# Kernel tuning notes

Measured on AMD Instinct MI355X. Metric: run time of the kernel, lower is better.

Reference implementation:

```python
import jax, jax.numpy as jnp
import numpy as np

B, N, D = 8, 128, 256
EPS = 1e-5


def _layernorm(x, g, b):
    m = jnp.mean(x, axis=-1, keepdims=True)
    v = jnp.mean(jnp.square(x - m), axis=-1, keepdims=True)
    return (x - m) * jax.lax.rsqrt(v + EPS) * g + b


def setup_inputs() -> dict:
    key = jax.random.key(0)
    ks = jax.random.split(key, 24)
    s = 0.05  # param init scale
    return {
        "text": jax.random.normal(ks[0], (B, N, D), jnp.float32),
        "adj1": jax.random.uniform(ks[1], (B, N, N), jnp.float32),
        "adj2": jax.random.uniform(ks[2], (B, N, N), jnp.float32),
        "edge1": jax.random.normal(ks[3], (B, N, N, D), jnp.float32) * 0.1,
        "edge2": jax.random.normal(ks[4], (B, N, N, D), jnp.float32) * 0.1,
        "textmask": jnp.ones((B, N), jnp.float32),
        "weight": jax.random.normal(ks[5], (D, D), jnp.float32) * s,
        "bias": jax.random.normal(ks[6], (D,), jnp.float32) * s,
        "gamma": jnp.ones((D,), jnp.float32),
        "beta": jnp.zeros((D,), jnp.float32),
        "fuse1_w": jax.random.normal(ks[7], (2 * D, D), jnp.float32) * s,
        "fuse2_w": jax.random.normal(ks[8], (2 * D, D), jnp.float32) * s,
        "fc3_w": jax.random.normal(ks[9], (2 * D, D), jnp.float32) * s,
        "fc1_w0": jax.random.normal(ks[10], (3 * D, D), jnp.float32) * s,
        "fc1_w1": jax.random.normal(ks[11], (D, 1), jnp.float32) * s,
        "fc1_b1": jnp.zeros((1,), jnp.float32),
        "fc2_w0": jax.random.normal(ks[12], (3 * D, D), jnp.float32) * s,
        "fc2_w1": jax.random.normal(ks[13], (D, 1), jnp.float32) * s,
        "fc2_b1": jnp.zeros((1,), jnp.float32),
        "align_lin": jax.random.normal(ks[14], (D, D), jnp.float32) * s,
        "align_bias": jax.random.normal(ks[15], (D,), jnp.float32) * s,
    }


def reference(text, adj1, adj2, edge1, edge2, textmask, weight, bias, gamma,
              beta, fuse1_w, fuse2_w, fc3_w, fc1_w0, fc1_w1, fc1_b1,
              fc2_w0, fc2_w1, fc2_b1, align_lin, align_bias):
    d = text.shape[-1]
    # ---- SelfAlignment ----
    logits = jnp.einsum('bid,bjd->bij', text @ align_lin, text)
    mask_add = (1.0 - textmask)[:, None, :] * -1e20
    probs = jax.nn.softmax(logits + mask_add, axis=-1)
    outss = jnp.einsum('bij,bjd->bid', probs, text) * textmask[..., None] + align_bias

    # ---- GCN body ----
    out = jax.nn.relu(text @ weight)  # [B,N,D]

    # edge contributions are loop-invariant: precompute once
    # torch cat([x,e]) @ W  ==  x @ W[:d] + e @ W[d:]
    e1_fuse = jnp.einsum('bijd,de->bije', edge1, fuse1_w[d:])
    e2_fuse = jnp.einsum('bijd,de->bije', edge2, fuse2_w[d:])
    e1_fc = jnp.einsum('bijd,de->bije', edge1, fc1_w0[2 * d:])
    e2_fc = jnp.einsum('bijd,de->bije', edge2, fc2_w0[2 * d:])

    denom1 = jnp.sum(adj1, axis=2, keepdims=True) + 1.0  # [B,N,1]
    denom2 = jnp.sum(adj2, axis=2, keepdims=True) + 1.0

    for _ in range(3):  # K = 3
        # text1[b,i,j] = out[b,i]; text2[b,i,j] = out[b,j]
        t_i1 = (out @ fc1_w0[:d])[:, :, None, :]        # text1 part, fc1
        t_j1 = (out @ fc1_w0[d:2 * d])[:, None, :, :]   # text2 part, fc1
        t_i2 = (out @ fc2_w0[:d])[:, :, None, :]
        t_j2 = (out @ fc2_w0[d:2 * d])[:, None, :, :]

        teout = jax.nn.relu((out @ fuse1_w[:d])[:, None, :, :] + e1_fuse)  # [B,N,N,D]
        tein = jax.nn.relu((out @ fuse2_w[:d])[:, None, :, :] + e2_fuse)

        s1 = jax.nn.sigmoid(jax.nn.relu(t_i1 + t_j1 + e1_fc) @ fc1_w1 + fc1_b1)[..., 0]  # [B,N,N]
        s2 = jax.nn.sigmoid(jax.nn.relu(t_i2 + t_j2 + e2_fc) @ fc2_w1 + fc2_b1)[..., 0]

        out1 = jnp.einsum('bij,bijd->bid', adj1 * s1, teout) / denom1
        out2 = jnp.einsum('bij,bijd->bid', adj2 * s2, tein) / denom2

        out = jax.nn.relu(out1 @ fc3_w[:d] + out2 @ fc3_w[d:]) + out + bias
        out = _layernorm(out, gamma, beta)  # dropout = identity (eval)
    return out, outss
```

## Files before the change

kernel.cpp:

```cpp
#include <hip/hip_runtime.h>

typedef unsigned short u16;
typedef unsigned int u32;
typedef __attribute__((ext_vector_type(8))) short bf16x8;
typedef __attribute__((ext_vector_type(4))) float f32x4;
typedef __attribute__((ext_vector_type(16))) float f32x16;

__device__ __forceinline__ u16 f2bf(float f) {
  u32 u = __float_as_uint(f);
  return (u16)((u + 0x7fffu + ((u >> 16) & 1u)) >> 16);
}
__device__ __forceinline__ float bf2f(u16 h) {
  return __uint_as_float(((u32)h) << 16);
}

__device__ __forceinline__ void glds16(const void* g, void* l) {
  __builtin_amdgcn_global_load_lds(
      (const __attribute__((address_space(1))) unsigned int*)g,
      (__attribute__((address_space(3))) unsigned int*)l, 16, 0, 0);
}

__device__ __forceinline__ f32x16 unpack16(const u16* p) {
  uint4 a = *(const uint4*)p, b = *(const uint4*)(p + 8);
  f32x16 r;
  r[0]  = __uint_as_float(a.x << 16); r[1]  = __uint_as_float(a.x & 0xffff0000u);
  r[2]  = __uint_as_float(a.y << 16); r[3]  = __uint_as_float(a.y & 0xffff0000u);
  r[4]  = __uint_as_float(a.z << 16); r[5]  = __uint_as_float(a.z & 0xffff0000u);
  r[6]  = __uint_as_float(a.w << 16); r[7]  = __uint_as_float(a.w & 0xffff0000u);
  r[8]  = __uint_as_float(b.x << 16); r[9]  = __uint_as_float(b.x & 0xffff0000u);
  r[10] = __uint_as_float(b.y << 16); r[11] = __uint_as_float(b.y & 0xffff0000u);
  r[12] = __uint_as_float(b.z << 16); r[13] = __uint_as_float(b.z & 0xffff0000u);
  r[14] = __uint_as_float(b.w << 16); r[15] = __uint_as_float(b.w & 0xffff0000u);
  return r;
}

__global__ __launch_bounds__(256) void convert_edge(
    const float* __restrict__ src, u16* __restrict__ dst) {
  int g = blockIdx.x * 256 + threadIdx.x;
  int kg = g & 7, r = (g >> 3) & 127, kc = (g >> 10) & 3, rt = g >> 12;
  const float* s = src + ((long)(rt * 128 + r) * 256 + kc * 64 + kg * 8);
  float4 a = *(const float4*)s, b = *(const float4*)(s + 4);
  ushort4 lo, hi;
  lo.x = f2bf(a.x); lo.y = f2bf(a.y); lo.z = f2bf(a.z); lo.w = f2bf(a.w);
  hi.x = f2bf(b.x); hi.y = f2bf(b.y); hi.z = f2bf(b.z); hi.w = f2bf(b.w);
  u16* d = dst + (long)rt * 65536 + kc * 16384 + r * 64 + (kg ^ (r & 7)) * 8;
  *(ushort4*)d = lo;
  *(ushort4*)(d + 4) = hi;
}

__global__ __launch_bounds__(256) void gemm_edge(
    const u16* __restrict__ A, const u16* __restrict__ Bt,
    u16* __restrict__ E) {
  __shared__ __align__(16) u16 Asm[8192];
  __shared__ __align__(16) u16 Bsm[8192];
  const int tid = threadIdx.x, lane = tid & 63, w = tid >> 6;
  const int m = lane & 15, q = lane >> 4;
  const int rt = blockIdx.x >> 2, ct = blockIdx.x & 3;
  const int wrow = (w & 1) * 64, wcol = (w >> 1) * 64;
  const char* Ab = (const char*)A + (long)rt * 131072;
  const char* Bb = (const char*)Bt + (long)ct * 65536;
  f32x4 acc[4][4];
#pragma unroll
  for (int r = 0; r < 4; ++r)
#pragma unroll
    for (int c = 0; c < 4; ++c) acc[r][c] = (f32x4){0.f, 0.f, 0.f, 0.f};

  for (int kc = 0; kc < 4; ++kc) {
#pragma unroll
    for (int t = 0; t < 4; ++t) {
      glds16(Ab + kc * 32768 + t * 4096 + tid * 16,
             (char*)Asm + t * 4096 + tid * 16);
      glds16(Bb + kc * 16384 + t * 4096 + tid * 16,
             (char*)Bsm + t * 4096 + tid * 16);
    }
    __syncthreads();
#pragma unroll
    for (int s = 0; s < 2; ++s) {
      const int ko2 = (s * 32 + q * 8) * 2;
      bf16x8 av[4], bv[4];
#pragma unroll
      for (int r = 0; r < 4; ++r) {
        int row = wrow + r * 16 + m;
        av[r] = *(const bf16x8*)((const char*)Asm + row * 128 +
                                 (ko2 ^ ((row & 7) * 16)));
      }
#pragma unroll
      for (int c = 0; c < 4; ++c) {
        int col = wcol + c * 16 + m;
        bv[c] = *(const bf16x8*)((const char*)Bsm + col * 128 +
                                 (ko2 ^ ((col & 7) * 16)));
      }
#pragma unroll
      for (int r = 0; r < 4; ++r)
#pragma unroll
        for (int c = 0; c < 4; ++c)
          acc[r][c] = __builtin_amdgcn_mfma_f32_16x16x32_bf16(
              av[r], bv[c], acc[r][c], 0, 0, 0);
    }
    __syncthreads();
  }
#pragma unroll
  for (int r = 0; r < 4; ++r)
#pragma unroll
    for (int c = 0; c < 4; ++c)
#pragma unroll
      for (int g = 0; g < 4; ++g) {
        long gr = (long)rt * 128 + wrow + r * 16 + q * 4 + g;
        int gc = ct * 128 + wcol + c * 16 + m;
        E[gr * 512 + gc] = f2bf(acc[r][c][g]);
      }
}

template<int K, int ROWS, bool OUT_BF16>
__global__ __launch_bounds__(256) void gemm_mfma(
    const float* __restrict__ A, const u16* __restrict__ Bt,
    void* __restrict__ Cv, int Ntot) {
  constexpr int LD = 72;
  constexpr int CF = (ROWS == 128) ? 8 : 4;
  __shared__ __align__(16) u16 Asm[ROWS * LD];
  __shared__ __align__(16) u16 Bsm[256 * LD];
  const int tid = threadIdx.x;
  const int lane = tid & 63;
  const int w = tid >> 6;
  const int m = lane & 15;
  const int q = lane >> 4;
  const int wrow = (ROWS == 128) ? (w & 1) * 64 : 0;
  const int wcol = (ROWS == 128) ? (w >> 1) * 128 : w * 64;
  const long rowbase = (long)blockIdx.x * ROWS;
  const long colbase = (long)blockIdx.y * 256;
  f32x4 acc[4][CF];
#pragma unroll
  for (int r = 0; r < 4; ++r)
#pragma unroll
    for (int c = 0; c < CF; ++c) acc[r][c] = (f32x4){0.f, 0.f, 0.f, 0.f};

  for (int kc = 0; kc < K / 64; ++kc) {
    const int kb = kc * 64;
#pragma unroll
    for (int it = 0; it < ROWS / 16; ++it) {
      int f = it * 256 + tid;
      int r = f >> 4, c4 = (f & 15) * 4;
      float4 v = *(const float4*)(A + (rowbase + r) * K + kb + c4);
      ushort4 h;
      h.x = f2bf(v.x); h.y = f2bf(v.y); h.z = f2bf(v.z); h.w = f2bf(v.w);
      *(ushort4*)&Asm[r * LD + c4] = h;
    }
#pragma unroll
    for (int it = 0; it < 8; ++it) {
      int f = it * 256 + tid;
      int c = f >> 3, k8 = (f & 7) * 8;
      *(uint4*)&Bsm[c * LD + k8] =
          *(const uint4*)(Bt + (colbase + c) * K + kb + k8);
    }
    __syncthreads();
#pragma unroll
    for (int s = 0; s < 2; ++s) {
      const int ko = s * 32 + q * 8;
      bf16x8 av[4], bv[CF];
#pragma unroll
      for (int r = 0; r < 4; ++r)
        av[r] = *(const bf16x8*)&Asm[(wrow + r * 16 + m) * LD + ko];
#pragma unroll
      for (int c = 0; c < CF; ++c)
        bv[c] = *(const bf16x8*)&Bsm[(wcol + c * 16 + m) * LD + ko];
#pragma unroll
      for (int r = 0; r < 4; ++r)
#pragma unroll
        for (int c = 0; c < CF; ++c)
          acc[r][c] = __builtin_amdgcn_mfma_f32_16x16x32_bf16(
              av[r], bv[c], acc[r][c], 0, 0, 0);
    }
    __syncthreads();
  }
#pragma unroll
  for (int r = 0; r < 4; ++r)
#pragma unroll
    for (int c = 0; c < CF; ++c)
#pragma unroll
      for (int g = 0; g < 4; ++g) {
        long gr = rowbase + wrow + r * 16 + q * 4 + g;
        long gc = colbase + wcol + c * 16 + m;
        float v = acc[r][c][g];
        if (OUT_BF16) ((u16*)Cv)[gr * Ntot + gc] = f2bf(v);
        else          ((float*)Cv)[gr * Ntot + gc] = v;
      }
}

__global__ __launch_bounds__(256) void prep_bt(
    const float* __restrict__ weight, const float* __restrict__ align_lin,
    const float* __restrict__ fuse1_w, const float* __restrict__ fuse2_w,
    const float* __restrict__ fc1_w0, const float* __restrict__ fc2_w0,
    const float* __restrict__ fc3_w,
    u16* BtE1, u16* BtE2, u16* BtW0, u16* BtLoop, u16* BtFc3) {
  int g = blockIdx.x * 256 + threadIdx.x;
  if (g < 262144) {
    int t = g & 131071;
    int col = t >> 8, k = t & 255;
    float v;
    if (g < 131072)
      v = (col < 256) ? fuse1_w[(256 + k) * 256 + col]
                      : fc1_w0[(512 + k) * 256 + (col - 256)];
    else
      v = (col < 256) ? fuse2_w[(256 + k) * 256 + col]
                      : fc2_w0[(512 + k) * 256 + (col - 256)];
    int ct = col >> 7, cc = col & 127, kc = k >> 6, kk = k & 63;
    u16* dst = (g < 131072) ? BtE1 : BtE2;
    dst[ct * 32768 + kc * 8192 + cc * 64 + (kk ^ ((cc & 7) * 8))] = f2bf(v);
  } else if (g < 393216) {
    int t = g - 262144;
    int c = t >> 8, k = t & 255;
    float v = (c < 256) ? weight[k * 256 + c] : align_lin[k * 256 + (c - 256)];
    BtW0[t] = f2bf(v);
  } else if (g < 786432) {
    int t = g - 393216;
    int c = t >> 8, k = t & 255;
    int seg = c >> 8, cc = c & 255;
    float v;
    if      (seg == 0) v = fuse1_w[k * 256 + cc];
    else if (seg == 1) v = fuse2_w[k * 256 + cc];
    else if (seg == 2) v = fc1_w0[k * 256 + cc];
    else if (seg == 3) v = fc1_w0[(256 + k) * 256 + cc];
    else if (seg == 4) v = fc2_w0[k * 256 + cc];
    else               v = fc2_w0[(256 + k) * 256 + cc];
    BtLoop[t] = f2bf(v);
  } else {
    int t = g - 786432;
    int c = t >> 9, k = t & 511;
    BtFc3[t] = f2bf(fc3_w[k * 256 + c]);
  }
}

__global__ __launch_bounds__(256) void relu0_kernel(const float* __restrict__ T0,
                                                    float* __restrict__ outb) {
  long r = blockIdx.x;
  int d = threadIdx.x;
  outb[r * 256 + d] = fmaxf(T0[r * 512 + d], 0.f);
}

__global__ __launch_bounds__(128) void align_kernel(
    const float* __restrict__ text, const float* __restrict__ T0,
    const float* __restrict__ textmask, const float* __restrict__ align_bias,
    float* __restrict__ outss) {
  const int bi = blockIdx.x;
  const int b = bi >> 7;
  const int tid = threadIdx.x;
  __shared__ float ta[256];
  __shared__ float pr[128];
  __shared__ float red[128];
  ta[tid]       = T0[(long)bi * 512 + 256 + tid];
  ta[tid + 128] = T0[(long)bi * 512 + 384 + tid];
  __syncthreads();
  const float* trow = text + (long)(b * 128 + tid) * 256;
  float dot = 0.f;
  for (int d = 0; d < 256; d += 4) {
    float4 t4 = *(const float4*)(trow + d);
    dot += t4.x * ta[d] + t4.y * ta[d + 1] + t4.z * ta[d + 2] + t4.w * ta[d + 3];
  }
  float logit = dot + (1.0f - textmask[b * 128 + tid]) * -1e20f;
  pr[tid] = logit;
  red[tid] = logit;
  __syncthreads();
  for (int off = 64; off; off >>= 1) {
    if (tid < off) red[tid] = fmaxf(red[tid], red[tid + off]);
    __syncthreads();
  }
  float mx = red[0];
  __syncthreads();
  float e = __expf(pr[tid] - mx);
  red[tid] = e;
  __syncthreads();
  for (int off = 64; off; off >>= 1) {
    if (tid < off) red[tid] += red[tid + off];
    __syncthreads();
  }
  float inv = 1.0f / red[0];
  __syncthreads();
  pr[tid] = e * inv;
  __syncthreads();
  const float mi = textmask[bi];
  for (int h = 0; h < 2; ++h) {
    int d = tid + h * 128;
    float s = 0.f;
    for (int j = 0; j < 128; ++j)
      s += pr[j] * text[(long)(b * 128 + j) * 256 + d];
    outss[(long)bi * 256 + d] = s * mi + align_bias[d];
  }
}

__global__ __launch_bounds__(256) void fused_gate(
    const u16* __restrict__ E1, const u16* __restrict__ E2,
    const float* __restrict__ P, const float* __restrict__ adj1,
    const float* __restrict__ adj2, const float* __restrict__ fc1w1,
    const float* __restrict__ fc1b1, const float* __restrict__ fc2w1,
    const float* __restrict__ fc2b1, float* __restrict__ OU12) {
  const int tid = threadIdx.x, lane = tid & 63, w = tid >> 6;
  const int g16 = lane >> 4, l16 = lane & 15;
  const int bi = blockIdx.x, b = bi >> 7;
  const int db = l16 * 16;
  const long rowi = (long)bi * 1536;
  const f32x16 w1v = *(const f32x16*)(fc1w1 + db);
  const f32x16 w2v = *(const f32x16*)(fc2w1 + db);
  const f32x16 ti1 = *(const f32x16*)(P + rowi + 512 + db);
  const f32x16 ti2 = *(const f32x16*)(P + rowi + 1024 + db);
  const float b1 = fc1b1[0], b2 = fc2b1[0];
  const long ebase = (long)bi * 65536;
  const int abase = bi * 128;
  f32x16 acc1, acc2;
#pragma unroll
  for (int dd = 0; dd < 16; ++dd) { acc1[dd] = 0.f; acc2[dd] = 0.f; }
  float da1 = 0.f, da2 = 0.f;

  for (int t = 0; t < 8; ++t) {
    const int j = w * 32 + t * 4 + g16;
    const long er = ebase + (long)j * 512;
    const long rowj = (long)(b * 128 + j) * 1536;
    f32x16 e1cf = unpack16(E1 + er + 256 + db);
    f32x16 e2cf = unpack16(E2 + er + 256 + db);
    f32x16 tj1 = *(const f32x16*)(P + rowj + 768 + db);
    f32x16 tj2 = *(const f32x16*)(P + rowj + 1280 + db);
    float a1 = adj1[abase + j], a2 = adj2[abase + j];
    float z1 = 0.f, z2 = 0.f;
#pragma unroll
    for (int dd = 0; dd < 16; ++dd) {
      z1 += fmaxf(ti1[dd] + tj1[dd] + e1cf[dd], 0.f) * w1v[dd];
      z2 += fmaxf(ti2[dd] + tj2[dd] + e2cf[dd], 0.f) * w2v[dd];
    }
#pragma unroll
    for (int off = 1; off < 16; off <<= 1) {
      z1 += __shfl_xor(z1, off);
      z2 += __shfl_xor(z2, off);
    }
    float s1 = a1 / (1.f + __expf(-(z1 + b1)));
    float s2 = a2 / (1.f + __expf(-(z2 + b2)));
    f32x16 e1ff = unpack16(E1 + er + db);
    f32x16 e2ff = unpack16(E2 + er + db);
    f32x16 of1 = *(const f32x16*)(P + rowj + db);
    f32x16 of2 = *(const f32x16*)(P + rowj + 256 + db);
#pragma unroll
    for (int dd = 0; dd < 16; ++dd) {
      acc1[dd] += s1 * fmaxf(of1[dd] + e1ff[dd], 0.f);
      acc2[dd] += s2 * fmaxf(of2[dd] + e2ff[dd], 0.f);
    }
    da1 += a1;
    da2 += a2;
  }

  __shared__ float redA[16][260];
  __shared__ float redB[16][260];
  __shared__ float dA[16], dB[16];
  const int p = w * 4 + g16;
#pragma unroll
  for (int v = 0; v < 4; ++v) {
    *(float4*)&redA[p][db + v * 4] =
        make_float4(acc1[v*4], acc1[v*4+1], acc1[v*4+2], acc1[v*4+3]);
    *(float4*)&redB[p][db + v * 4] =
        make_float4(acc2[v*4], acc2[v*4+1], acc2[v*4+2], acc2[v*4+3]);
  }
  if (l16 == 0) { dA[p] = da1; dB[p] = da2; }
  __syncthreads();
  float o1 = 0.f, o2 = 0.f, d1 = 1.f, d2 = 1.f;
#pragma unroll
  for (int pp = 0; pp < 16; ++pp) {
    o1 += redA[pp][tid];
    o2 += redB[pp][tid];
    d1 += dA[pp];
    d2 += dB[pp];
  }
  OU12[(long)bi * 512 + tid] = o1 / d1;
  OU12[(long)bi * 512 + 256 + tid] = o2 / d2;
}

__global__ __launch_bounds__(256) void ln_kernel(
    const float* __restrict__ Y, const float* __restrict__ prev,
    const float* __restrict__ bias, const float* __restrict__ gamma,
    const float* __restrict__ beta, float* __restrict__ dst) {
  const int row = blockIdx.x, tid = threadIdx.x, lane = tid & 63, w = tid >> 6;
  const long idx = (long)row * 256 + tid;
  float v = fmaxf(Y[idx], 0.f) + prev[idx] + bias[tid];
  float s = v;
#pragma unroll
  for (int off = 32; off; off >>= 1) s += __shfl_xor(s, off);
  __shared__ float wsA[4], wsB[4];
  if (lane == 0) wsA[w] = s;
  __syncthreads();
  float mean = (wsA[0] + wsA[1] + wsA[2] + wsA[3]) * (1.0f / 256.0f);
  float c = v - mean;
  float s2 = c * c;
#pragma unroll
  for (int off = 32; off; off >>= 1) s2 += __shfl_xor(s2, off);
  if (lane == 0) wsB[w] = s2;
  __syncthreads();
  float var = (wsB[0] + wsB[1] + wsB[2] + wsB[3]) * (1.0f / 256.0f);
  dst[idx] = c * rsqrtf(var + 1e-5f) * gamma[tid] + beta[tid];
}

extern "C" void kernel_launch(void* const* d_in, const int* in_sizes, int n_in,
                              void* d_out, int out_size, void* d_ws, size_t ws_size,
                              hipStream_t stream) {
  const float* text      = (const float*)d_in[0];
  const float* adj1      = (const float*)d_in[1];
  const float* adj2      = (const float*)d_in[2];
  const float* edge1     = (const float*)d_in[3];
  const float* edge2     = (const float*)d_in[4];
  const float* textmask  = (const float*)d_in[5];
  const float* weight    = (const float*)d_in[6];
  const float* bias      = (const float*)d_in[7];
  const float* gamma     = (const float*)d_in[8];
  const float* beta      = (const float*)d_in[9];
  const float* fuse1_w   = (const float*)d_in[10];
  const float* fuse2_w   = (const float*)d_in[11];
  const float* fc3_w     = (const float*)d_in[12];
  const float* fc1_w0    = (const float*)d_in[13];
  const float* fc1_w1    = (const float*)d_in[14];
  const float* fc1_b1    = (const float*)d_in[15];
  const float* fc2_w0    = (const float*)d_in[16];
  const float* fc2_w1    = (const float*)d_in[17];
  const float* fc2_b1    = (const float*)d_in[18];
  const float* align_lin = (const float*)d_in[19];
  const float* align_bias= (const float*)d_in[20];
  float* outF = (float*)d_out;

  char* w8 = (char*)d_ws;
  u16* Ax   = (u16*)w8;
  u16* E1   = (u16*)(w8 + 67108864);
  u16* E2   = (u16*)(w8 + 201326592);
  u16* BtE1 = (u16*)(w8 + 335544320);
  u16* BtE2 = BtE1 + 131072;
  u16* BtW0 = BtE2 + 131072;
  u16* BtLoop = BtW0 + 131072;
  u16* BtFc3  = BtLoop + 393216;
  float* P    = (float*)w8;
  float* T0   = P + 1572864;
  float* OU12 = T0 + 524288;
  float* outb = OU12 + 524288;
  float* Yb   = outb + 262144;

  prep_bt<<<3584, 256, 0, stream>>>(weight, align_lin, fuse1_w, fuse2_w,
                                    fc1_w0, fc2_w0, fc3_w,
                                    BtE1, BtE2, BtW0, BtLoop, BtFc3);
  convert_edge<<<16384, 256, 0, stream>>>(edge1, Ax);
  gemm_edge<<<4096, 256, 0, stream>>>(Ax, BtE1, E1);
  convert_edge<<<16384, 256, 0, stream>>>(edge2, Ax);
  gemm_edge<<<4096, 256, 0, stream>>>(Ax, BtE2, E2);
  gemm_mfma<256, 64, false><<<dim3(16, 2), 256, 0, stream>>>(text, BtW0, T0, 512);
  relu0_kernel<<<1024, 256, 0, stream>>>(T0, outb);
  align_kernel<<<1024, 128, 0, stream>>>(text, T0, textmask, align_bias,
                                         outF + 262144);
  for (int it = 0; it < 3; ++it) {
    gemm_mfma<256, 64, false><<<dim3(16, 6), 256, 0, stream>>>(outb, BtLoop, P, 1536);
    fused_gate<<<1024, 256, 0, stream>>>(E1, E2, P, adj1, adj2, fc1_w1, fc1_b1,
                                         fc2_w1, fc2_b1, OU12);
    gemm_mfma<512, 64, false><<<dim3(16, 1), 256, 0, stream>>>(OU12, BtFc3, Yb, 256);
    ln_kernel<<<1024, 256, 0, stream>>>(Yb, outb, bias, gamma, beta,
                                        (it == 2) ? outF : outb);
  }
}
```

Measured before the change: 767.3 us.

## Shrink GEMM row tiles, fuse relu0 into GEMM, split gate into two phases

The small-GEMM template now takes its row count as RF fragments of 16 rows, and calls use 32-row tiles with twice as many blocks, spreading the tiny GEMMs over more CUs. The standalone relu0 kernel is removed; the first GEMM writes the ReLU of its first 256 columns directly, saving one launch. fused_gate is split into two phases: the gate scalars for all j go into shared memory first, then the message accumulation runs, with a shuffle-based reduction, smaller shared buffers, and the adjacency row-sum computed once per block. In exchange, each GEMM block gets less A-tile reuse and the gate kernel gains an extra barrier.

```diff
diff --git a/kernel.cpp b/kernel.cpp
--- a/kernel.cpp
+++ b/kernel.cpp
@@ -111,12 +111,12 @@
       }
 }
 
-template<int K, int ROWS, bool OUT_BF16>
+template<int K, int RF, bool OUT_BF16, bool RELU0>
 __global__ __launch_bounds__(256) void gemm_mfma(
     const float* __restrict__ A, const u16* __restrict__ Bt,
-    void* __restrict__ Cv, int Ntot) {
+    void* __restrict__ Cv, int Ntot, float* __restrict__ relu_dst) {
+  constexpr int ROWS = RF * 16;
   constexpr int LD = 72;
-  constexpr int CF = (ROWS == 128) ? 8 : 4;
   __shared__ __align__(16) u16 Asm[ROWS * LD];
   __shared__ __align__(16) u16 Bsm[256 * LD];
   const int tid = threadIdx.x;
@@ -124,20 +124,19 @@
   const int w = tid >> 6;
   const int m = lane & 15;
   const int q = lane >> 4;
-  const int wrow = (ROWS == 128) ? (w & 1) * 64 : 0;
-  const int wcol = (ROWS == 128) ? (w >> 1) * 128 : w * 64;
+  const int wcol = w * 64;
   const long rowbase = (long)blockIdx.x * ROWS;
   const long colbase = (long)blockIdx.y * 256;
-  f32x4 acc[4][CF];
-#pragma unroll
-  for (int r = 0; r < 4; ++r)
-#pragma unroll
-    for (int c = 0; c < CF; ++c) acc[r][c] = (f32x4){0.f, 0.f, 0.f, 0.f};
+  f32x4 acc[RF][4];
+#pragma unroll
+  for (int r = 0; r < RF; ++r)
+#pragma unroll
+    for (int c = 0; c < 4; ++c) acc[r][c] = (f32x4){0.f, 0.f, 0.f, 0.f};
 
   for (int kc = 0; kc < K / 64; ++kc) {
     const int kb = kc * 64;
 #pragma unroll
-    for (int it = 0; it < ROWS / 16; ++it) {
+    for (int it = 0; it < RF; ++it) {
       int f = it * 256 + tid;
       int r = f >> 4, c4 = (f & 15) * 4;
       float4 v = *(const float4*)(A + (rowbase + r) * K + kb + c4);
@@ -156,33 +155,36 @@
 #pragma unroll
     for (int s = 0; s < 2; ++s) {
       const int ko = s * 32 + q * 8;
-      bf16x8 av[4], bv[CF];
-#pragma unroll
-      for (int r = 0; r < 4; ++r)
-        av[r] = *(const bf16x8*)&Asm[(wrow + r * 16 + m) * LD + ko];
-#pragma unroll
-      for (int c = 0; c < CF; ++c)
+      bf16x8 av[RF], bv[4];
+#pragma unroll
+      for (int r = 0; r < RF; ++r)
+        av[r] = *(const bf16x8*)&Asm[(r * 16 + m) * LD + ko];
+#pragma unroll
+      for (int c = 0; c < 4; ++c)
         bv[c] = *(const bf16x8*)&Bsm[(wcol + c * 16 + m) * LD + ko];
 #pragma unroll
-      for (int r = 0; r < 4; ++r)
-#pragma unroll
-        for (int c = 0; c < CF; ++c)
+      for (int r = 0; r < RF; ++r)
+#pragma unroll
+        for (int c = 0; c < 4; ++c)
           acc[r][c] = __builtin_amdgcn_mfma_f32_16x16x32_bf16(
               av[r], bv[c], acc[r][c], 0, 0, 0);
     }
     __syncthreads();
   }
 #pragma unroll
-  for (int r = 0; r < 4; ++r)
-#pragma unroll
-    for (int c = 0; c < CF; ++c)
+  for (int r = 0; r < RF; ++r)
+#pragma unroll
+    for (int c = 0; c < 4; ++c)
 #pragma unroll
       for (int g = 0; g < 4; ++g) {
-        long gr = rowbase + wrow + r * 16 + q * 4 + g;
+        long gr = rowbase + r * 16 + q * 4 + g;
         long gc = colbase + wcol + c * 16 + m;
         float v = acc[r][c][g];
         if (OUT_BF16) ((u16*)Cv)[gr * Ntot + gc] = f2bf(v);
         else          ((float*)Cv)[gr * Ntot + gc] = v;
+        if (RELU0) {
+          if (gc < 256) relu_dst[gr * 256 + gc] = fmaxf(v, 0.f);
+        }
       }
 }
 
@@ -230,13 +232,6 @@
   }
 }
 
-__global__ __launch_bounds__(256) void relu0_kernel(const float* __restrict__ T0,
-                                                    float* __restrict__ outb) {
-  long r = blockIdx.x;
-  int d = threadIdx.x;
-  outb[r * 256 + d] = fmaxf(T0[r * 512 + d], 0.f);
-}
-
 __global__ __launch_bounds__(128) void align_kernel(
     const float* __restrict__ text, const float* __restrict__ T0,
     const float* __restrict__ textmask, const float* __restrict__ align_bias,
@@ -298,76 +293,93 @@
   const int bi = blockIdx.x, b = bi >> 7;
   const int db = l16 * 16;
   const long rowi = (long)bi * 1536;
-  const f32x16 w1v = *(const f32x16*)(fc1w1 + db);
-  const f32x16 w2v = *(const f32x16*)(fc2w1 + db);
-  const f32x16 ti1 = *(const f32x16*)(P + rowi + 512 + db);
-  const f32x16 ti2 = *(const f32x16*)(P + rowi + 1024 + db);
-  const float b1 = fc1b1[0], b2 = fc2b1[0];
   const long ebase = (long)bi * 65536;
   const int abase = bi * 128;
+
+  __shared__ float sA[128], sB[128];
+  __shared__ float redA[4][256], redB[4][256];
+  __shared__ float dInv[2];
+
+  if (w < 2) {
+    const float* adj = w ? adj2 : adj1;
+    float v = adj[abase + lane] + adj[abase + 64 + lane];
+#pragma unroll
+    for (int off = 32; off; off >>= 1) v += __shfl_xor(v, off);
+    if (lane == 0) dInv[w] = 1.f / (1.f + v);
+  }
+
+  {
+    const f32x16 w1v = *(const f32x16*)(fc1w1 + db);
+    const f32x16 w2v = *(const f32x16*)(fc2w1 + db);
+    const f32x16 ti1 = *(const f32x16*)(P + rowi + 512 + db);
+    const f32x16 ti2 = *(const f32x16*)(P + rowi + 1024 + db);
+    const float b1 = fc1b1[0], b2 = fc2b1[0];
+#pragma unroll
+    for (int t = 0; t < 8; ++t) {
+      const int j = w * 32 + t * 4 + g16;
+      const long er = ebase + (long)j * 512;
+      const long rowj = (long)((b << 7) + j) * 1536;
+      f32x16 e1 = unpack16(E1 + er + 256 + db);
+      f32x16 e2 = unpack16(E2 + er + 256 + db);
+      f32x16 t1 = *(const f32x16*)(P + rowj + 768 + db);
+      f32x16 t2 = *(const f32x16*)(P + rowj + 1280 + db);
+      float z1 = 0.f, z2 = 0.f;
+#pragma unroll
+      for (int dd = 0; dd < 16; ++dd) {
+        z1 += fmaxf(ti1[dd] + t1[dd] + e1[dd], 0.f) * w1v[dd];
+        z2 += fmaxf(ti2[dd] + t2[dd] + e2[dd], 0.f) * w2v[dd];
+      }
+#pragma unroll
+      for (int off = 1; off < 16; off <<= 1) {
+        z1 += __shfl_xor(z1, off);
+        z2 += __shfl_xor(z2, off);
+      }
+      if (l16 == 0) {
+        sA[j] = adj1[abase + j] / (1.f + __expf(-(z1 + b1)));
+        sB[j] = adj2[abase + j] / (1.f + __expf(-(z2 + b2)));
+      }
+    }
+  }
+  __syncthreads();
+
   f32x16 acc1, acc2;
 #pragma unroll
   for (int dd = 0; dd < 16; ++dd) { acc1[dd] = 0.f; acc2[dd] = 0.f; }
-  float da1 = 0.f, da2 = 0.f;
-
+#pragma unroll
   for (int t = 0; t < 8; ++t) {
     const int j = w * 32 + t * 4 + g16;
     const long er = ebase + (long)j * 512;
-    const long rowj = (long)(b * 128 + j) * 1536;
-    f32x16 e1cf = unpack16(E1 + er + 256 + db);
-    f32x16 e2cf = unpack16(E2 + er + 256 + db);
-    f32x16 tj1 = *(const f32x16*)(P + rowj + 768 + db);
-    f32x16 tj2 = *(const f32x16*)(P + rowj + 1280 + db);
-    float a1 = adj1[abase + j], a2 = adj2[abase + j];
-    float z1 = 0.f, z2 = 0.f;
+    const long rowj = (long)((b << 7) + j) * 1536;
+    f32x16 e1 = unpack16(E1 + er + db);
+    f32x16 e2 = unpack16(E2 + er + db);
+    f32x16 o1 = *(const f32x16*)(P + rowj + db);
+    f32x16 o2 = *(const f32x16*)(P + rowj + 256 + db);
+    const float s1 = sA[j], s2 = sB[j];
 #pragma unroll
     for (int dd = 0; dd < 16; ++dd) {
-      z1 += fmaxf(ti1[dd] + tj1[dd] + e1cf[dd], 0.f) * w1v[dd];
-      z2 += fmaxf(ti2[dd] + tj2[dd] + e2cf[dd], 0.f) * w2v[dd];
-    }
-#pragma unroll
-    for (int off = 1; off < 16; off <<= 1) {
-      z1 += __shfl_xor(z1, off);
-      z2 += __shfl_xor(z2, off);
-    }
-    float s1 = a1 / (1.f + __expf(-(z1 + b1)));
-    float s2 = a2 / (1.f + __expf(-(z2 + b2)));
-    f32x16 e1ff = unpack16(E1 + er + db);
-    f32x16 e2ff = unpack16(E2 + er + db);
-    f32x16 of1 = *(const f32x16*)(P + rowj + db);
-    f32x16 of2 = *(const f32x16*)(P + rowj + 256 + db);
-#pragma unroll
-    for (int dd = 0; dd < 16; ++dd) {
-      acc1[dd] += s1 * fmaxf(of1[dd] + e1ff[dd], 0.f);
-      acc2[dd] += s2 * fmaxf(of2[dd] + e2ff[dd], 0.f);
-    }
-    da1 += a1;
-    da2 += a2;
-  }
-
-  __shared__ float redA[16][260];
-  __shared__ float redB[16][260];
-  __shared__ float dA[16], dB[16];
-  const int p = w * 4 + g16;
-#pragma unroll
-  for (int v = 0; v < 4; ++v) {
-    *(float4*)&redA[p][db + v * 4] =
-        make_float4(acc1[v*4], acc1[v*4+1], acc1[v*4+2], acc1[v*4+3]);
-    *(float4*)&redB[p][db + v * 4] =
-        make_float4(acc2[v*4], acc2[v*4+1], acc2[v*4+2], acc2[v*4+3]);
-  }
-  if (l16 == 0) { dA[p] = da1; dB[p] = da2; }
-  __syncthreads();
-  float o1 = 0.f, o2 = 0.f, d1 = 1.f, d2 = 1.f;
-#pragma unroll
-  for (int pp = 0; pp < 16; ++pp) {
-    o1 += redA[pp][tid];
-    o2 += redB[pp][tid];
-    d1 += dA[pp];
-    d2 += dB[pp];
-  }
-  OU12[(long)bi * 512 + tid] = o1 / d1;
-  OU12[(long)bi * 512 + 256 + tid] = o2 / d2;
+      acc1[dd] += s1 * fmaxf(o1[dd] + e1[dd], 0.f);
+      acc2[dd] += s2 * fmaxf(o2[dd] + e2[dd], 0.f);
+    }
+  }
+
+#pragma unroll
+  for (int dd = 0; dd < 16; ++dd) {
+    float a = acc1[dd], c = acc2[dd];
+    a += __shfl_xor(a, 16); a += __shfl_xor(a, 32);
+    c += __shfl_xor(c, 16); c += __shfl_xor(c, 32);
+    acc1[dd] = a; acc2[dd] = c;
+  }
+  *(float4*)&redA[w][db + g16 * 4] =
+      make_float4(acc1[g16 * 4], acc1[g16 * 4 + 1],
+                  acc1[g16 * 4 + 2], acc1[g16 * 4 + 3]);
+  *(float4*)&redB[w][db + g16 * 4] =
+      make_float4(acc2[g16 * 4], acc2[g16 * 4 + 1],
+                  acc2[g16 * 4 + 2], acc2[g16 * 4 + 3]);
+  __syncthreads();
+  float o1 = redA[0][tid] + redA[1][tid] + redA[2][tid] + redA[3][tid];
+  float o2 = redB[0][tid] + redB[1][tid] + redB[2][tid] + redB[3][tid];
+  OU12[(long)bi * 512 + tid] = o1 * dInv[0];
+  OU12[(long)bi * 512 + 256 + tid] = o2 * dInv[1];
 }
 
 __global__ __launch_bounds__(256) void ln_kernel(
@@ -442,15 +454,17 @@
   gemm_edge<<<4096, 256, 0, stream>>>(Ax, BtE1, E1);
   convert_edge<<<16384, 256, 0, stream>>>(edge2, Ax);
   gemm_edge<<<4096, 256, 0, stream>>>(Ax, BtE2, E2);
-  gemm_mfma<256, 64, false><<<dim3(16, 2), 256, 0, stream>>>(text, BtW0, T0, 512);
-  relu0_kernel<<<1024, 256, 0, stream>>>(T0, outb);
+  gemm_mfma<256, 2, false, true><<<dim3(32, 2), 256, 0, stream>>>(
+      text, BtW0, T0, 512, outb);
   align_kernel<<<1024, 128, 0, stream>>>(text, T0, textmask, align_bias,
                                          outF + 262144);
   for (int it = 0; it < 3; ++it) {
-    gemm_mfma<256, 64, false><<<dim3(16, 6), 256, 0, stream>>>(outb, BtLoop, P, 1536);
+    gemm_mfma<256, 2, false, false><<<dim3(32, 6), 256, 0, stream>>>(
+        outb, BtLoop, P, 1536, nullptr);
     fused_gate<<<1024, 256, 0, stream>>>(E1, E2, P, adj1, adj2, fc1_w1, fc1_b1,
                                          fc2_w1, fc2_b1, OU12);
-    gemm_mfma<512, 64, false><<<dim3(16, 1), 256, 0, stream>>>(OU12, BtFc3, Yb, 256);
+    gemm_mfma<512, 2, false, false><<<dim3(32, 1), 256, 0, stream>>>(
+        OU12, BtFc3, Yb, 256, nullptr);
     ln_kernel<<<1024, 256, 0, stream>>>(Yb, outb, bias, gamma, beta,
                                         (it == 2) ? outF : outb);
   }
```

New measurement: 843.4 us. 9.9% more time.
